# Performance work log

Hardware: AMD Instinct MI355X
Metric: run time of the kernel (lower is better)

## Reference

```python
import jax, jax.numpy as jnp
import numpy as np
from jax import lax

I, H, O, T = 256, 1024, 1, 16384

def setup_inputs() -> dict:
    key = jax.random.key(0)
    ks = jax.random.split(key, 10)
    k = 1.0 / np.sqrt(H)
    u = lambda kk, shp, lim: jax.random.uniform(kk, shp, jnp.float32, -lim, lim)
    return {
        "input_seq": jax.random.normal(ks[0], (1, T, I), jnp.float32),
        # LSTM params (PyTorch layout: [4H, in], gate order i,f,g,o)
        "W_ih": u(ks[1], (4 * H, I), k),
        "W_hh": u(ks[2], (4 * H, H), k),
        "b_ih": u(ks[3], (4 * H,), k),
        "b_hh": u(ks[4], (4 * H,), k),
        # MLP head: Linear(H,H) -> ReLU -> Linear(H,O)
        "W1": u(ks[5], (H, H), k),
        "b1": u(ks[6], (H,), k),
        "W2": u(ks[7], (O, H), k),
        "b2": u(ks[8], (O,), k),
    }

def reference(input_seq, W_ih, W_hh, b_ih, b_hh, W1, b1, W2, b2):
    x = input_seq[0]                       # [T, I] (batch must be 1, see forward's h.reshape(1,-1))
    # Precompute input contribution to gates for all timesteps in one GEMM.
    xg = x @ W_ih.T + (b_ih + b_hh)        # [T, 4H]

    def step(carry, xg_t):
        h, c = carry                       # [H], [H]
        g = xg_t + h @ W_hh.T              # [4H]
        i, f, gg, o = jnp.split(g, 4)
        i = jax.nn.sigmoid(i)
        f = jax.nn.sigmoid(f)
        gg = jnp.tanh(gg)
        o = jax.nn.sigmoid(o)
        c = f * c + i * gg
        h = o * jnp.tanh(c)
        return (h, c), None

    h0 = jnp.zeros((H,), dtype=x.dtype)
    c0 = jnp.zeros((H,), dtype=x.dtype)
    (h, c), _ = lax.scan(step, (h0, c0), xg)

    hflat = h[None, :]                     # h.reshape(1, -1) with B=1 -> [1, H]
    z = jax.nn.relu(hflat @ W1.T + b1)     # [1, H]
    return z @ W2.T + b2                   # [1, O]
```

## Files before the change

kernel.cpp:

```cpp
#include <hip/hip_runtime.h>
#include <cstdint>

#define I_DIM   256
#define H_DIM   1024
#define T_STEPS 16384
#define NBLK    128
#define CELLS   8
#define THREADS 512

__launch_bounds__(THREADS, 2)
__global__ void lstm_persist(const float* __restrict__ x,
                             const float* __restrict__ W_ih,
                             const float* __restrict__ W_hh,
                             const float* __restrict__ b_ih,
                             const float* __restrict__ b_hh,
                             unsigned long long* __restrict__ ring)
{
    __shared__ __align__(16) float h_cur[H_DIM];
    __shared__ __align__(16) float xbuf[2][I_DIM];

    const int tid = threadIdx.x;
    const int blk = blockIdx.x;
    const int wv  = tid >> 6;
    const int q   = (tid >> 4) & 3;
    const int l   = tid & 15;
    const int row_g = q * H_DIM + blk * CELLS + wv;

    float4 w4[16];
    {
        const float4* Wrow = reinterpret_cast<const float4*>(W_hh + (size_t)row_g * H_DIM);
        #pragma unroll
        for (int jj = 0; jj < 16; ++jj) w4[jj] = Wrow[jj * 16 + l];
    }
    float4 wih4[4];
    {
        const float4* Wrow = reinterpret_cast<const float4*>(W_ih + (size_t)row_g * I_DIM);
        #pragma unroll
        for (int s = 0; s < 4; ++s) wih4[s] = Wrow[s * 16 + l];
    }
    const float bias_r = b_ih[row_g] + b_hh[row_g];

    if (tid < 64)
        *reinterpret_cast<float4*>(&xbuf[0][tid * 4]) =
            *reinterpret_cast<const float4*>(x + tid * 4);
    __syncthreads();

    float xg = (l == 0) ? bias_r : 0.f;
    #pragma unroll
    for (int s = 0; s < 4; ++s) {
        const float4 xv = *reinterpret_cast<const float4*>(&xbuf[0][s * 64 + l * 4]);
        xg += wih4[s].x * xv.x + wih4[s].y * xv.y + wih4[s].z * xv.z + wih4[s].w * xv.w;
    }

    if (tid < 64)
        *reinterpret_cast<float4*>(&xbuf[1][tid * 4]) =
            *reinterpret_cast<const float4*>(x + I_DIM + tid * 4);
    int   cur     = 1;
    float c_state = 0.f;

    for (int t = 0; t < T_STEPS; ++t) {
        float4 xpre;
        if (tid < 64) {
            const int tt = (t + 2 < T_STEPS) ? t + 2 : T_STEPS - 1;
            xpre = *reinterpret_cast<const float4*>(x + (size_t)tt * I_DIM + tid * 4);
        }
        float2 hv;
        if (t == 0) {
            hv.x = 0.f; hv.y = 0.f;
        } else {
            const unsigned long long want = (unsigned long long)(t - 1);
            unsigned long long* p = ring + (((t - 1) & 1) ? H_DIM : 0) + 2 * tid;
            unsigned long long v0 = 0, v1 = 0;
            bool g0 = false, g1 = false;
            do {
                if (!g0) { v0 = __hip_atomic_load(p,     __ATOMIC_RELAXED, __HIP_MEMORY_SCOPE_AGENT); g0 = ((v0 >> 32) == want); }
                if (!g1) { v1 = __hip_atomic_load(p + 1, __ATOMIC_RELAXED, __HIP_MEMORY_SCOPE_AGENT); g1 = ((v1 >> 32) == want); }
            } while (!(g0 && g1));
            hv.x = __uint_as_float((unsigned)v0);
            hv.y = __uint_as_float((unsigned)v1);
        }
        *reinterpret_cast<float2*>(&h_cur[2 * tid]) = hv;
        __syncthreads();

        float acc = xg;
        #pragma unroll
        for (int jj = 0; jj < 16; ++jj) {
            const float4 h4 = *reinterpret_cast<const float4*>(&h_cur[jj * 64 + l * 4]);
            acc += w4[jj].x * h4.x + w4[jj].y * h4.y + w4[jj].z * h4.z + w4[jj].w * h4.w;
        }
        acc += __shfl_xor(acc, 1);
        acc += __shfl_xor(acc, 2);
        acc += __shfl_xor(acc, 4);
        acc += __shfl_xor(acc, 8);
        const float gi_r = __shfl(acc, 0);
        const float gf_r = __shfl(acc, 16);
        const float gg_r = __shfl(acc, 32);
        const float go_r = __shfl(acc, 48);
        const float gi = 1.f / (1.f + expf(-gi_r));
        const float gf = 1.f / (1.f + expf(-gf_r));
        const float gg = tanhf(gg_r);
        const float go = 1.f / (1.f + expf(-go_r));
        c_state = gf * c_state + gi * gg;
        const float h_new = go * tanhf(c_state);
        if ((tid & 63) == 0) {
            const unsigned long long pack =
                ((unsigned long long)t << 32) | (unsigned long long)__float_as_uint(h_new);
            __hip_atomic_store(ring + ((t & 1) ? H_DIM : 0) + blk * CELLS + wv, pack,
                               __ATOMIC_RELAXED, __HIP_MEMORY_SCOPE_AGENT);
        }

        float xg_n = (l == 0) ? bias_r : 0.f;
        #pragma unroll
        for (int s = 0; s < 4; ++s) {
            const float4 xv = *reinterpret_cast<const float4*>(&xbuf[cur][s * 64 + l * 4]);
            xg_n += wih4[s].x * xv.x + wih4[s].y * xv.y + wih4[s].z * xv.z + wih4[s].w * xv.w;
        }
        xg = xg_n;
        __syncthreads();
        if (tid < 64)
            *reinterpret_cast<float4*>(&xbuf[cur ^ 1][tid * 4]) = xpre;
        cur ^= 1;
    }
}

__global__ void ffn_kernel(const unsigned long long* __restrict__ ring,
                           const float* __restrict__ W1,
                           const float* __restrict__ b1,
                           const float* __restrict__ W2,
                           float* __restrict__ partials)
{
    __shared__ float psum[8];
    const int tid = threadIdx.x;
    const int r2  = tid >> 5;
    const int l2  = tid & 31;
    const int j   = blockIdx.x * 8 + r2;
    const unsigned long long* hslot = ring + (((T_STEPS - 1) & 1) ? H_DIM : 0);

    float acc = 0.f;
    #pragma unroll 8
    for (int kk = 0; kk < 32; ++kk) {
        const int   k  = kk * 32 + l2;
        const float hk = __uint_as_float((unsigned)hslot[k]);
        acc += hk * W1[(size_t)j * H_DIM + k];
    }
    acc += __shfl_xor(acc, 1);
    acc += __shfl_xor(acc, 2);
    acc += __shfl_xor(acc, 4);
    acc += __shfl_xor(acc, 8);
    acc += __shfl_xor(acc, 16);
    if (l2 == 0) {
        float z = acc + b1[j];
        z = z > 0.f ? z : 0.f;
        psum[r2] = z * W2[j];
    }
    __syncthreads();
    if (tid == 0) {
        float s = 0.f;
        #pragma unroll
        for (int i = 0; i < 8; ++i) s += psum[i];
        partials[blockIdx.x] = s;
    }
}

__global__ void out_kernel(const float* __restrict__ partials,
                           const float* __restrict__ b2,
                           float* __restrict__ out)
{
    __shared__ float ws2[2];
    const int tid = threadIdx.x;
    float v = partials[tid];
    v += __shfl_xor(v, 1);
    v += __shfl_xor(v, 2);
    v += __shfl_xor(v, 4);
    v += __shfl_xor(v, 8);
    v += __shfl_xor(v, 16);
    v += __shfl_xor(v, 32);
    if ((tid & 63) == 0) ws2[tid >> 6] = v;
    __syncthreads();
    if (tid == 0) out[0] = ws2[0] + ws2[1] + b2[0];
}

extern "C" void kernel_launch(void* const* d_in, const int* in_sizes, int n_in,
                              void* d_out, int out_size, void* d_ws, size_t ws_size,
                              hipStream_t stream)
{
    const float* x    = (const float*)d_in[0];
    const float* W_ih = (const float*)d_in[1];
    const float* W_hh = (const float*)d_in[2];
    const float* b_ih = (const float*)d_in[3];
    const float* b_hh = (const float*)d_in[4];
    const float* W1   = (const float*)d_in[5];
    const float* b1   = (const float*)d_in[6];
    const float* W2   = (const float*)d_in[7];
    const float* b2   = (const float*)d_in[8];
    float* out = (float*)d_out;

    unsigned long long* ring = (unsigned long long*)d_ws;
    const size_t ring_bytes = (size_t)2 * H_DIM * sizeof(unsigned long long);
    float* partials = (float*)((char*)d_ws + ring_bytes);

    hipMemsetAsync(d_ws, 0xAA, ring_bytes, stream);

    lstm_persist<<<NBLK, THREADS, 0, stream>>>(x, W_ih, W_hh, b_ih, b_hh, ring);
    ffn_kernel<<<128, 256, 0, stream>>>(ring, W1, b1, W2, partials);
    out_kernel<<<1, 128, 0, stream>>>(partials, b2, out);
}
```

Before: 34.52 ms.

## Double-buffer hidden state to drop second barrier, use fast activations

Double-buffers the shared hidden-state array so the second __syncthreads per timestep can be removed, and moves the x prefetch store into the window after the first barrier. Replaces expf/tanhf with __expf plus a hardware reciprocal, adds s_sleep to the spin-wait, changes launch bounds to 1 block per CU, and manually unrolls the weight registers. The aim is shorter latency on each step of the serial recurrence. Removing the barrier depends on the next step's spin-wait barrier protecting buffer reuse, and the fast math loses some precision. The s_sleep may add wake-up latency to the spin.

```diff
diff --git a/kernel.cpp b/kernel.cpp
--- a/kernel.cpp
+++ b/kernel.cpp
@@ -8,7 +8,17 @@
 #define CELLS   8
 #define THREADS 512
 
-__launch_bounds__(THREADS, 2)
+__device__ __forceinline__ float fast_sigmoid(float x) {
+    return __builtin_amdgcn_rcpf(1.f + __expf(-x));
+}
+__device__ __forceinline__ float fast_tanh(float x) {
+    const float a = fabsf(x);
+    const float e = __expf(-2.f * a);
+    const float t = (1.f - e) * __builtin_amdgcn_rcpf(1.f + e);
+    return copysignf(t, x);
+}
+
+__launch_bounds__(THREADS, 1)
 __global__ void lstm_persist(const float* __restrict__ x,
                              const float* __restrict__ W_ih,
                              const float* __restrict__ W_hh,
@@ -16,7 +26,7 @@
                              const float* __restrict__ b_hh,
                              unsigned long long* __restrict__ ring)
 {
-    __shared__ __align__(16) float h_cur[H_DIM];
+    __shared__ __align__(16) float h_cur[2][H_DIM];
     __shared__ __align__(16) float xbuf[2][I_DIM];
 
     const int tid = threadIdx.x;
@@ -26,18 +36,13 @@
     const int l   = tid & 15;
     const int row_g = q * H_DIM + blk * CELLS + wv;
 
-    float4 w4[16];
-    {
-        const float4* Wrow = reinterpret_cast<const float4*>(W_hh + (size_t)row_g * H_DIM);
-        #pragma unroll
-        for (int jj = 0; jj < 16; ++jj) w4[jj] = Wrow[jj * 16 + l];
-    }
-    float4 wih4[4];
-    {
-        const float4* Wrow = reinterpret_cast<const float4*>(W_ih + (size_t)row_g * I_DIM);
-        #pragma unroll
-        for (int s = 0; s < 4; ++s) wih4[s] = Wrow[s * 16 + l];
-    }
+    const float4* Wrow = reinterpret_cast<const float4*>(W_hh + (size_t)row_g * H_DIM);
+    float4 wA0  = Wrow[ 0*16 + l], wA1  = Wrow[ 1*16 + l], wA2  = Wrow[ 2*16 + l], wA3  = Wrow[ 3*16 + l];
+    float4 wA4  = Wrow[ 4*16 + l], wA5  = Wrow[ 5*16 + l], wA6  = Wrow[ 6*16 + l], wA7  = Wrow[ 7*16 + l];
+    float4 wA8  = Wrow[ 8*16 + l], wA9  = Wrow[ 9*16 + l], wA10 = Wrow[10*16 + l], wA11 = Wrow[11*16 + l];
+    float4 wA12 = Wrow[12*16 + l], wA13 = Wrow[13*16 + l], wA14 = Wrow[14*16 + l], wA15 = Wrow[15*16 + l];
+    const float4* Vrow = reinterpret_cast<const float4*>(W_ih + (size_t)row_g * I_DIM);
+    float4 wI0 = Vrow[0*16 + l], wI1 = Vrow[1*16 + l], wI2 = Vrow[2*16 + l], wI3 = Vrow[3*16 + l];
     const float bias_r = b_ih[row_g] + b_hh[row_g];
 
     if (tid < 64)
@@ -45,12 +50,20 @@
             *reinterpret_cast<const float4*>(x + tid * 4);
     __syncthreads();
 
+#define XG_DOT(dst, buf)                                                              \
+    {                                                                                 \
+        const float4 x0 = *reinterpret_cast<const float4*>(&(buf)[0 * 64 + l * 4]);   \
+        const float4 x1 = *reinterpret_cast<const float4*>(&(buf)[1 * 64 + l * 4]);   \
+        const float4 x2 = *reinterpret_cast<const float4*>(&(buf)[2 * 64 + l * 4]);   \
+        const float4 x3 = *reinterpret_cast<const float4*>(&(buf)[3 * 64 + l * 4]);   \
+        dst += wI0.x * x0.x + wI0.y * x0.y + wI0.z * x0.z + wI0.w * x0.w;             \
+        dst += wI1.x * x1.x + wI1.y * x1.y + wI1.z * x1.z + wI1.w * x1.w;             \
+        dst += wI2.x * x2.x + wI2.y * x2.y + wI2.z * x2.z + wI2.w * x2.w;             \
+        dst += wI3.x * x3.x + wI3.y * x3.y + wI3.z * x3.z + wI3.w * x3.w;             \
+    }
+
     float xg = (l == 0) ? bias_r : 0.f;
-    #pragma unroll
-    for (int s = 0; s < 4; ++s) {
-        const float4 xv = *reinterpret_cast<const float4*>(&xbuf[0][s * 64 + l * 4]);
-        xg += wih4[s].x * xv.x + wih4[s].y * xv.y + wih4[s].z * xv.z + wih4[s].w * xv.w;
-    }
+    XG_DOT(xg, xbuf[0]);
 
     if (tid < 64)
         *reinterpret_cast<float4*>(&xbuf[1][tid * 4]) =
@@ -72,22 +85,34 @@
             unsigned long long* p = ring + (((t - 1) & 1) ? H_DIM : 0) + 2 * tid;
             unsigned long long v0 = 0, v1 = 0;
             bool g0 = false, g1 = false;
-            do {
+            for (;;) {
                 if (!g0) { v0 = __hip_atomic_load(p,     __ATOMIC_RELAXED, __HIP_MEMORY_SCOPE_AGENT); g0 = ((v0 >> 32) == want); }
                 if (!g1) { v1 = __hip_atomic_load(p + 1, __ATOMIC_RELAXED, __HIP_MEMORY_SCOPE_AGENT); g1 = ((v1 >> 32) == want); }
-            } while (!(g0 && g1));
+                if (g0 && g1) break;
+                __builtin_amdgcn_s_sleep(1);
+            }
             hv.x = __uint_as_float((unsigned)v0);
             hv.y = __uint_as_float((unsigned)v1);
         }
-        *reinterpret_cast<float2*>(&h_cur[2 * tid]) = hv;
+        float* hb = h_cur[t & 1];
+        *reinterpret_cast<float2*>(&hb[2 * tid]) = hv;
         __syncthreads();
 
+        if (tid < 64)
+            *reinterpret_cast<float4*>(&xbuf[cur ^ 1][tid * 4]) = xpre;
+
         float acc = xg;
-        #pragma unroll
-        for (int jj = 0; jj < 16; ++jj) {
-            const float4 h4 = *reinterpret_cast<const float4*>(&h_cur[jj * 64 + l * 4]);
-            acc += w4[jj].x * h4.x + w4[jj].y * h4.y + w4[jj].z * h4.z + w4[jj].w * h4.w;
-        }
+#define HDOT(J, WREG)                                                                 \
+        {                                                                             \
+            const float4 h4 = *reinterpret_cast<const float4*>(&hb[(J) * 64 + l * 4]);\
+            acc += WREG.x * h4.x + WREG.y * h4.y + WREG.z * h4.z + WREG.w * h4.w;     \
+        }
+        HDOT( 0, wA0)  HDOT( 1, wA1)  HDOT( 2, wA2)  HDOT( 3, wA3)
+        HDOT( 4, wA4)  HDOT( 5, wA5)  HDOT( 6, wA6)  HDOT( 7, wA7)
+        HDOT( 8, wA8)  HDOT( 9, wA9)  HDOT(10, wA10) HDOT(11, wA11)
+        HDOT(12, wA12) HDOT(13, wA13) HDOT(14, wA14) HDOT(15, wA15)
+#undef HDOT
+
         acc += __shfl_xor(acc, 1);
         acc += __shfl_xor(acc, 2);
         acc += __shfl_xor(acc, 4);
@@ -96,12 +121,12 @@
         const float gf_r = __shfl(acc, 16);
         const float gg_r = __shfl(acc, 32);
         const float go_r = __shfl(acc, 48);
-        const float gi = 1.f / (1.f + expf(-gi_r));
-        const float gf = 1.f / (1.f + expf(-gf_r));
-        const float gg = tanhf(gg_r);
-        const float go = 1.f / (1.f + expf(-go_r));
+        const float gi = fast_sigmoid(gi_r);
+        const float gf = fast_sigmoid(gf_r);
+        const float gg = fast_tanh(gg_r);
+        const float go = fast_sigmoid(go_r);
         c_state = gf * c_state + gi * gg;
-        const float h_new = go * tanhf(c_state);
+        const float h_new = go * fast_tanh(c_state);
         if ((tid & 63) == 0) {
             const unsigned long long pack =
                 ((unsigned long long)t << 32) | (unsigned long long)__float_as_uint(h_new);
@@ -110,17 +135,11 @@
         }
 
         float xg_n = (l == 0) ? bias_r : 0.f;
-        #pragma unroll
-        for (int s = 0; s < 4; ++s) {
-            const float4 xv = *reinterpret_cast<const float4*>(&xbuf[cur][s * 64 + l * 4]);
-            xg_n += wih4[s].x * xv.x + wih4[s].y * xv.y + wih4[s].z * xv.z + wih4[s].w * xv.w;
-        }
+        XG_DOT(xg_n, xbuf[cur]);
         xg = xg_n;
-        __syncthreads();
-        if (tid < 64)
-            *reinterpret_cast<float4*>(&xbuf[cur ^ 1][tid * 4]) = xpre;
         cur ^= 1;
     }
+#undef XG_DOT
 }
 
 __global__ void ffn_kernel(const unsigned long long* __restrict__ ring,
```

Result: slower. 53.33 ms (+54.5%).
